# Kernel optimization log

Measured on AMD Instinct MI355X. Metric: run time of the kernel, lower is better.

## Reference

```python
import jax, jax.numpy as jnp
import numpy as np

# Module constants (match init_kwargs)
H = 16            # num_heads
K = 64            # max_kernel_size
MAX_FREQ = 16.0
MIN_FREQ = 1.0
HALF_S = 16       # int(32**(1/1)) // 2
S = 2 * HALF_S + 1  # 33 sample offsets: -16..16
MAX_RECEPTIVE = HALF_S * MAX_FREQ  # 256.0


def setup_inputs() -> dict:
    key = jax.random.key(0)
    ks = jax.random.split(key, 6)
    B, L, C = 1, 4096, 1024
    x = jax.random.normal(ks[0], (B, L, C), dtype=jnp.float32)
    # Learned params (random small scale so offsets/kernels vary; torch inits
    # wave_proj to zeros but that degenerates the math under test).
    Ww = jax.random.normal(ks[1], (2 * H, C), dtype=jnp.float32) * 0.02
    bw = jnp.zeros((2 * H,), dtype=jnp.float32)
    Wk = jax.random.normal(ks[2], (H * K, C), dtype=jnp.float32) * 0.02
    bk = jnp.zeros((H * K,), dtype=jnp.float32)
    Wo = jax.random.normal(ks[3], (C, C), dtype=jnp.float32) * 0.02
    return {"x": x, "Ww": Ww, "bw": bw, "Wk": Wk, "bk": bk, "Wo": Wo}


def reference(x, Ww, bw, Wk, bk, Wo):
    B, L, C = x.shape
    D = C // H
    dt = x.dtype
    grid = jnp.arange(-HALF_S, HALF_S + 1, dtype=dt)  # (S,)

    # Predict per-position frequency / phase (averaged over heads)
    wp = jax.nn.silu(x @ Ww.T + bw).reshape(B, L, 2, H)
    freq = jax.nn.sigmoid(wp[:, :, 0]) * (MAX_FREQ - MIN_FREQ) + MIN_FREQ  # (B,L,H)
    phase = jnp.tanh(wp[:, :, 1]) * MAX_FREQ
    freq_avg = freq.mean(-1)    # (B,L)
    phase_avg = phase.mean(-1)  # (B,L)

    # Sample positions & gather indices
    rel_pos = grid[None, None, :] * freq_avg[..., None] + phase_avg[..., None]  # (B,L,S)
    centers = jnp.arange(L, dtype=dt)
    sample_pos = centers[None, :, None] + rel_pos                               # (B,L,S)
    valid = (sample_pos >= 0) & (sample_pos < L)
    sample_idx = jnp.clip(sample_pos.astype(jnp.int32), 0, L - 1)               # trunc toward 0, like torch .long()

    # Gather values: (B,L,S,C) -> (B,L,H,S,D)
    values = jax.vmap(lambda xf, idx: xf[idx])(x, sample_idx)
    values = values.reshape(B, L, S, H, D).transpose(0, 1, 3, 2, 4)

    # Kernel profile, linearly interpolated to sample positions
    kernel_max = jax.nn.silu(x @ Wk.T + bk).reshape(B, L, H, K)
    norm_pos = jnp.clip((rel_pos + MAX_RECEPTIVE) / (2.0 * MAX_RECEPTIVE), 0.0, 1.0)
    idx_float = norm_pos * (K - 1)                       # (B,L,S)
    idx_floor = jnp.clip(idx_float.astype(jnp.int32), 0, K - 2)
    w_ceil = (idx_float - idx_floor.astype(dt))[:, :, None, :]  # (B,L,1,S)
    w_floor = 1.0 - w_ceil
    ifl = jnp.broadcast_to(idx_floor[:, :, None, :], (B, L, H, S))
    k_floor = jnp.take_along_axis(kernel_max, ifl, axis=-1)
    k_ceil = jnp.take_along_axis(kernel_max, ifl + 1, axis=-1)
    kernel = (k_floor * w_floor + k_ceil * w_ceil) * valid[:, :, None, :].astype(dt)
    kernel = kernel / (kernel.sum(-1, keepdims=True) + 1e-8)

    out = jnp.einsum('blhsd,blhs->blhd', values, kernel).reshape(B, L, C)
    out = jax.nn.silu(out @ Wo.T)
    return out
```

## Files before the change

kernel.cpp:

```cpp
#include <hip/hip_runtime.h>
#include <math.h>

#define LDIM 4096
#define CDIM 1024
#define HDIM 16
#define KDIM 64
#define SDIM 33
#define HALF_SS 16
#define MAXF 16.0f
#define MINF 1.0f
#define MAXR 256.0f

typedef double d4 __attribute__((ext_vector_type(4)));

#define MFMA_F64 __builtin_amdgcn_mfma_f64_16x16x4f64

__device__ __forceinline__ float sigmoid_np(float z) {
  float e = (float)exp(-(double)z);
  return __fdiv_rn(1.0f, __fadd_rn(1.0f, e));
}
__device__ __forceinline__ float silu_f(float z) {
  return __fmul_rn(z, sigmoid_np(z));
}

__device__ __forceinline__ float np_pairwise_sum(const float* a, int n) {
  float r[8];
#pragma unroll
  for (int j = 0; j < 8; ++j) r[j] = a[j];
  int i = 8;
  for (; i + 8 <= n; i += 8)
#pragma unroll
    for (int j = 0; j < 8; ++j) r[j] = __fadd_rn(r[j], a[i + j]);
  float res = __fadd_rn(__fadd_rn(__fadd_rn(r[0], r[1]), __fadd_rn(r[2], r[3])),
                        __fadd_rn(__fadd_rn(r[4], r[5]), __fadd_rn(r[6], r[7])));
  for (; i < n; ++i) res = __fadd_rn(res, a[i]);
  return res;
}

__global__ __launch_bounds__(256) void wave_kernel(
    const float* __restrict__ x, const float* __restrict__ Ww,
    const float* __restrict__ bw, float* __restrict__ fa, float* __restrict__ pa) {
  __shared__ float xs[CDIM];
  __shared__ float wp[2 * HDIM];
  int l = blockIdx.x;
  int tid = threadIdx.x;
  const float* xrow = x + (size_t)l * CDIM;
  for (int c = tid; c < CDIM; c += 256) xs[c] = xrow[c];
  __syncthreads();
  int j = tid >> 3, sub = tid & 7;
  const float* wrow = Ww + j * CDIM;
  double acc = 0.0;
  for (int c = sub; c < CDIM; c += 8) acc += (double)xs[c] * (double)wrow[c];
  for (int off = 4; off; off >>= 1) acc += __shfl_down(acc, off, 8);
  if (sub == 0) {
    float v32 = (float)(acc + (double)bw[j]);
    wp[j] = silu_f(v32);
  }
  __syncthreads();
  if (tid == 0) {
    float fv[HDIM], pv[HDIM];
    for (int h = 0; h < HDIM; ++h) {
      fv[h] = __fadd_rn(__fmul_rn(sigmoid_np(wp[h]), MAXF - MINF), MINF);
      float t32 = (float)tanh((double)wp[HDIM + h]);
      pv[h] = __fmul_rn(t32, MAXF);
    }
    fa[l] = __fdiv_rn(np_pairwise_sum(fv, HDIM), (float)HDIM);
    pa[l] = __fdiv_rn(np_pairwise_sum(pv, HDIM), (float)HDIM);
  }
}

__global__ __launch_bounds__(256) void gemm_bt_silu_f64(
    const float* __restrict__ A, const float* __restrict__ B,
    const float* __restrict__ bias, float* __restrict__ Cout,
    int M, int N, int Kd) {
  __shared__ float Asf[128][36];
  __shared__ float Bsf[64][36];
  int tid = threadIdx.x;
  int w  = tid >> 6;
  int l  = tid & 63;
  int m0 = blockIdx.y * 128, n0 = blockIdx.x * 64;

  d4 zv = (d4)(0.0);
  double lane_d = (double)l;
  d4 pA = MFMA_F64(lane_d, 1.0, zv, 0, 0, 0);
  d4 pB = MFMA_F64(1.0, lane_d, zv, 0, 0, 0);
  int sa0 = (int)pA[0], sb0 = (int)pB[0];
  bool aH1 = ((sa0 & 3) == 0);
  bool bH1 = ((sb0 & 3) == 0);
  int lmA = aH1 ? (l & 15) : (l >> 2);
  int lqA = aH1 ? (l >> 4) : (l & 3);
  int lmB = bH1 ? (l & 15) : (l >> 2);
  int lqB = bH1 ? (l >> 4) : (l & 3);
  int di[4], dj[4];
#pragma unroll
  for (int r = 0; r < 4; ++r) {
    int va = (int)pA[r], vb = (int)pB[r];
    di[r] = (aH1 ? ((va - 96) >> 2) : ((va - 6) >> 4)) & 15;
    dj[r] = (bH1 ? ((vb - 96) >> 2) : ((vb - 6) >> 4)) & 15;
  }

  d4 acc[8];
#pragma unroll
  for (int i = 0; i < 8; ++i) acc[i] = (d4)(0.0);

  for (int kt = 0; kt < Kd; kt += 32) {
#pragma unroll
    for (int qi = 0; qi < 4; ++qi) {
      int e = tid + 256 * qi;
      int row = e >> 3, j = e & 7;
      float4 v = *(const float4*)(A + (size_t)(m0 + row) * Kd + kt + 4 * j);
      Asf[row][j] = v.x; Asf[row][j + 8] = v.y;
      Asf[row][j + 16] = v.z; Asf[row][j + 24] = v.w;
    }
#pragma unroll
    for (int qi = 0; qi < 2; ++qi) {
      int e = tid + 256 * qi;
      int row = e >> 3, j = e & 7;
      float4 v = *(const float4*)(B + (size_t)(n0 + row) * Kd + kt + 4 * j);
      Bsf[row][j] = v.x; Bsf[row][j + 8] = v.y;
      Bsf[row][j + 16] = v.z; Bsf[row][j + 24] = v.w;
    }
    __syncthreads();
#pragma unroll
    for (int t = 0; t < 2; ++t) {
      float4 bv = *(const float4*)&Bsf[16 * w + lmB][8 * lqB + 4 * t];
      float4 av0 = *(const float4*)&Asf[lmA][8 * lqA + 4 * t];
      float4 av1 = *(const float4*)&Asf[16 + lmA][8 * lqA + 4 * t];
      float4 av2 = *(const float4*)&Asf[32 + lmA][8 * lqA + 4 * t];
      float4 av3 = *(const float4*)&Asf[48 + lmA][8 * lqA + 4 * t];
      float4 av4 = *(const float4*)&Asf[64 + lmA][8 * lqA + 4 * t];
      float4 av5 = *(const float4*)&Asf[80 + lmA][8 * lqA + 4 * t];
      float4 av6 = *(const float4*)&Asf[96 + lmA][8 * lqA + 4 * t];
      float4 av7 = *(const float4*)&Asf[112 + lmA][8 * lqA + 4 * t];
      float bs[4] = {bv.x, bv.y, bv.z, bv.w};
      float as0[4] = {av0.x, av0.y, av0.z, av0.w};
      float as1[4] = {av1.x, av1.y, av1.z, av1.w};
      float as2[4] = {av2.x, av2.y, av2.z, av2.w};
      float as3[4] = {av3.x, av3.y, av3.z, av3.w};
      float as4[4] = {av4.x, av4.y, av4.z, av4.w};
      float as5[4] = {av5.x, av5.y, av5.z, av5.w};
      float as6[4] = {av6.x, av6.y, av6.z, av6.w};
      float as7[4] = {av7.x, av7.y, av7.z, av7.w};
#pragma unroll
      for (int s = 0; s < 4; ++s) {
        double bd = (double)bs[s];
        acc[0] = MFMA_F64((double)as0[s], bd, acc[0], 0, 0, 0);
        acc[1] = MFMA_F64((double)as1[s], bd, acc[1], 0, 0, 0);
        acc[2] = MFMA_F64((double)as2[s], bd, acc[2], 0, 0, 0);
        acc[3] = MFMA_F64((double)as3[s], bd, acc[3], 0, 0, 0);
        acc[4] = MFMA_F64((double)as4[s], bd, acc[4], 0, 0, 0);
        acc[5] = MFMA_F64((double)as5[s], bd, acc[5], 0, 0, 0);
        acc[6] = MFMA_F64((double)as6[s], bd, acc[6], 0, 0, 0);
        acc[7] = MFMA_F64((double)as7[s], bd, acc[7], 0, 0, 0);
      }
    }
    __syncthreads();
  }

#pragma unroll
  for (int mt = 0; mt < 8; ++mt) {
#pragma unroll
    for (int r = 0; r < 4; ++r) {
      int mm = m0 + 16 * mt + di[r];
      int nn = n0 + 16 * w + dj[r];
      float v32 = (float)acc[mt][r];
      v32 = __fadd_rn(v32, bias[nn]);
      Cout[(size_t)mm * N + nn] = silu_f(v32);
    }
  }
}

__global__ __launch_bounds__(256) void gemm_bt_silu_f32(
    const float* __restrict__ A, const float* __restrict__ B,
    float* __restrict__ Cout, int M, int N, int Kd) {
  __shared__ float Asf[16][128];
  __shared__ float Bsf[16][128];
  int tid = threadIdx.x;
  int tx = tid & 15, ty = tid >> 4;
  int m0 = blockIdx.y * 128, n0 = blockIdx.x * 128;
  float acc[8][8] = {};
  for (int kt = 0; kt < Kd; kt += 16) {
#pragma unroll
    for (int q = 0; q < 2; ++q) {
      int e = tid + 256 * q;
      int row = e >> 2, kq = (e & 3) * 4;
      float4 va = *(const float4*)(A + (size_t)(m0 + row) * Kd + kt + kq);
      Asf[kq + 0][row] = va.x; Asf[kq + 1][row] = va.y;
      Asf[kq + 2][row] = va.z; Asf[kq + 3][row] = va.w;
      float4 vb = *(const float4*)(B + (size_t)(n0 + row) * Kd + kt + kq);
      Bsf[kq + 0][row] = vb.x; Bsf[kq + 1][row] = vb.y;
      Bsf[kq + 2][row] = vb.z; Bsf[kq + 3][row] = vb.w;
    }
    __syncthreads();
#pragma unroll
    for (int kk = 0; kk < 16; ++kk) {
      float4 a0 = *(const float4*)&Asf[kk][ty * 8];
      float4 a1 = *(const float4*)&Asf[kk][ty * 8 + 4];
      float4 b0 = *(const float4*)&Bsf[kk][tx * 8];
      float4 b1 = *(const float4*)&Bsf[kk][tx * 8 + 4];
      float a[8] = {a0.x, a0.y, a0.z, a0.w, a1.x, a1.y, a1.z, a1.w};
      float b[8] = {b0.x, b0.y, b0.z, b0.w, b1.x, b1.y, b1.z, b1.w};
#pragma unroll
      for (int i = 0; i < 8; ++i)
#pragma unroll
        for (int j2 = 0; j2 < 8; ++j2) acc[i][j2] += a[i] * b[j2];
    }
    __syncthreads();
  }
#pragma unroll
  for (int i = 0; i < 8; ++i) {
    int mm = m0 + ty * 8 + i;
#pragma unroll
    for (int j2 = 0; j2 < 8; ++j2) {
      int nn = n0 + tx * 8 + j2;
      Cout[(size_t)mm * N + nn] = silu_f(acc[i][j2]);
    }
  }
}

__global__ __launch_bounds__(256) void conv_kernel(
    const float* __restrict__ x, const float* __restrict__ km,
    const float* __restrict__ fa, const float* __restrict__ pa,
    float* __restrict__ conv) {
  int l = blockIdx.x;
  int tid = threadIdx.x;
  __shared__ int s_idx[SDIM];
  __shared__ int s_ifl[SDIM];
  __shared__ float s_wc[SDIM];
  __shared__ float s_val[SDIM];
  __shared__ float kern[HDIM][SDIM];
  __shared__ float s_den[HDIM];
  if (tid < SDIM) {
    float f = fa[l], p = pa[l];
    float rel = __fadd_rn(__fmul_rn((float)(tid - HALF_SS), f), p);
    float pos = __fadd_rn((float)l, rel);
    bool valid = (pos >= 0.f) && (pos < (float)LDIM);
    int idx = (int)pos;
    idx = min(max(idx, 0), LDIM - 1);
    s_idx[tid] = idx;
    s_val[tid] = valid ? 1.f : 0.f;
    float np_ = __fdiv_rn(__fadd_rn(rel, MAXR), 2.f * MAXR);
    np_ = fminf(fmaxf(np_, 0.f), 1.f);
    float idxf = __fmul_rn(np_, (float)(KDIM - 1));
    int ifl = (int)idxf;
    ifl = min(max(ifl, 0), KDIM - 2);
    s_ifl[tid] = ifl;
    s_wc[tid] = __fsub_rn(idxf, (float)ifl);
  }
  __syncthreads();
  for (int t = tid; t < HDIM * SDIM; t += 256) {
    int h = t / SDIM, s = t - h * SDIM;
    const float* kb = km + (size_t)l * CDIM + h * KDIM;
    float wc = s_wc[s];
    float wf = __fsub_rn(1.f, wc);
    float v = __fadd_rn(__fmul_rn(kb[s_ifl[s]], wf), __fmul_rn(kb[s_ifl[s] + 1], wc));
    kern[h][s] = __fmul_rn(v, s_val[s]);
  }
  __syncthreads();
  if (tid < HDIM) {
    float sum = np_pairwise_sum(&kern[tid][0], SDIM);
    s_den[tid] = __fadd_rn(sum, 1e-8f);
  }
  __syncthreads();
  for (int t = tid; t < HDIM * SDIM; t += 256) {
    int h = t / SDIM, s = t - h * SDIM;
    kern[h][s] = __fdiv_rn(kern[h][s], s_den[h]);
  }
  __syncthreads();
  float acc[4] = {0.f, 0.f, 0.f, 0.f};
  for (int s = 0; s < SDIM; ++s) {
    const float* xr = x + (size_t)s_idx[s] * CDIM;
#pragma unroll
    for (int q = 0; q < 4; ++q) {
      int c = tid + q * 256;
      acc[q] = __fadd_rn(acc[q], __fmul_rn(xr[c], kern[c >> 6][s]));
    }
  }
#pragma unroll
  for (int q = 0; q < 4; ++q) {
    int c = tid + q * 256;
    conv[(size_t)l * CDIM + c] = acc[q];
  }
}

extern "C" void kernel_launch(void* const* d_in, const int* in_sizes, int n_in,
                              void* d_out, int out_size, void* d_ws, size_t ws_size,
                              hipStream_t stream) {
  const float* x  = (const float*)d_in[0];
  const float* Ww = (const float*)d_in[1];
  const float* bw = (const float*)d_in[2];
  const float* Wk = (const float*)d_in[3];
  const float* bk = (const float*)d_in[4];
  const float* Wo = (const float*)d_in[5];
  float* out = (float*)d_out;

  float* fa   = (float*)d_ws;
  float* pa   = fa + LDIM;
  float* km   = pa + LDIM;
  float* conv = km + (size_t)LDIM * CDIM;

  wave_kernel<<<LDIM, 256, 0, stream>>>(x, Ww, bw, fa, pa);

  dim3 kmgrid(CDIM / 64, LDIM / 128);
  gemm_bt_silu_f64<<<kmgrid, 256, 0, stream>>>(x, Wk, bk, km, LDIM, CDIM, CDIM);

  conv_kernel<<<LDIM, 256, 0, stream>>>(x, km, fa, pa, conv);

  dim3 ogrid(CDIM / 128, LDIM / 128);
  gemm_bt_silu_f32<<<ogrid, 256, 0, stream>>>(conv, Wo, out, LDIM, CDIM, CDIM);
}
```

Baseline: 456.1 us.

## Retile output GEMM to 512 threads, pad LDS, vectorize conv loads and stores

```diff
diff --git a/kernel.cpp b/kernel.cpp
--- a/kernel.cpp
+++ b/kernel.cpp
@@ -170,51 +170,51 @@
   }
 }
 
-__global__ __launch_bounds__(256) void gemm_bt_silu_f32(
+__global__ __launch_bounds__(512) void gemm_bt_silu_f32(
     const float* __restrict__ A, const float* __restrict__ B,
     float* __restrict__ Cout, int M, int N, int Kd) {
-  __shared__ float Asf[16][128];
-  __shared__ float Bsf[16][128];
+  __shared__ float Asf[16][132];
+  __shared__ float Bsf[16][132];
   int tid = threadIdx.x;
-  int tx = tid & 15, ty = tid >> 4;
+  int tx = tid & 15;
+  int ty = tid >> 4;
   int m0 = blockIdx.y * 128, n0 = blockIdx.x * 128;
-  float acc[8][8] = {};
+  float acc[4][8] = {};
+  int rS = tid >> 2, kq = (tid & 3) * 4;
   for (int kt = 0; kt < Kd; kt += 16) {
-#pragma unroll
-    for (int q = 0; q < 2; ++q) {
-      int e = tid + 256 * q;
-      int row = e >> 2, kq = (e & 3) * 4;
-      float4 va = *(const float4*)(A + (size_t)(m0 + row) * Kd + kt + kq);
-      Asf[kq + 0][row] = va.x; Asf[kq + 1][row] = va.y;
-      Asf[kq + 2][row] = va.z; Asf[kq + 3][row] = va.w;
-      float4 vb = *(const float4*)(B + (size_t)(n0 + row) * Kd + kt + kq);
-      Bsf[kq + 0][row] = vb.x; Bsf[kq + 1][row] = vb.y;
-      Bsf[kq + 2][row] = vb.z; Bsf[kq + 3][row] = vb.w;
+    {
+      float4 va = *(const float4*)(A + (size_t)(m0 + rS) * Kd + kt + kq);
+      Asf[kq + 0][rS] = va.x; Asf[kq + 1][rS] = va.y;
+      Asf[kq + 2][rS] = va.z; Asf[kq + 3][rS] = va.w;
+      float4 vb = *(const float4*)(B + (size_t)(n0 + rS) * Kd + kt + kq);
+      Bsf[kq + 0][rS] = vb.x; Bsf[kq + 1][rS] = vb.y;
+      Bsf[kq + 2][rS] = vb.z; Bsf[kq + 3][rS] = vb.w;
     }
     __syncthreads();
 #pragma unroll
     for (int kk = 0; kk < 16; ++kk) {
-      float4 a0 = *(const float4*)&Asf[kk][ty * 8];
-      float4 a1 = *(const float4*)&Asf[kk][ty * 8 + 4];
-      float4 b0 = *(const float4*)&Bsf[kk][tx * 8];
-      float4 b1 = *(const float4*)&Bsf[kk][tx * 8 + 4];
-      float a[8] = {a0.x, a0.y, a0.z, a0.w, a1.x, a1.y, a1.z, a1.w};
+      float4 a0 = *(const float4*)&Asf[kk][ty * 4];
+      float4 b0 = *(const float4*)&Bsf[kk][tx * 4];
+      float4 b1 = *(const float4*)&Bsf[kk][tx * 4 + 64];
+      float a[4] = {a0.x, a0.y, a0.z, a0.w};
       float b[8] = {b0.x, b0.y, b0.z, b0.w, b1.x, b1.y, b1.z, b1.w};
 #pragma unroll
-      for (int i = 0; i < 8; ++i)
+      for (int i = 0; i < 4; ++i)
 #pragma unroll
         for (int j2 = 0; j2 < 8; ++j2) acc[i][j2] += a[i] * b[j2];
     }
     __syncthreads();
   }
 #pragma unroll
-  for (int i = 0; i < 8; ++i) {
-    int mm = m0 + ty * 8 + i;
-#pragma unroll
-    for (int j2 = 0; j2 < 8; ++j2) {
-      int nn = n0 + tx * 8 + j2;
-      Cout[(size_t)mm * N + nn] = silu_f(acc[i][j2]);
-    }
+  for (int i = 0; i < 4; ++i) {
+    int mm = m0 + ty * 4 + i;
+    float4 o0, o1;
+    o0.x = silu_f(acc[i][0]); o0.y = silu_f(acc[i][1]);
+    o0.z = silu_f(acc[i][2]); o0.w = silu_f(acc[i][3]);
+    o1.x = silu_f(acc[i][4]); o1.y = silu_f(acc[i][5]);
+    o1.z = silu_f(acc[i][6]); o1.w = silu_f(acc[i][7]);
+    *(float4*)&Cout[(size_t)mm * N + n0 + 4 * tx] = o0;
+    *(float4*)&Cout[(size_t)mm * N + n0 + 64 + 4 * tx] = o1;
   }
 }
 
@@ -222,7 +222,8 @@
     const float* __restrict__ x, const float* __restrict__ km,
     const float* __restrict__ fa, const float* __restrict__ pa,
     float* __restrict__ conv) {
-  int l = blockIdx.x;
+  int bid = blockIdx.x;
+  int l = (bid & 7) * (LDIM / 8) + (bid >> 3);
   int tid = threadIdx.x;
   __shared__ int s_idx[SDIM];
   __shared__ int s_ifl[SDIM];
@@ -267,20 +268,20 @@
     kern[h][s] = __fdiv_rn(kern[h][s], s_den[h]);
   }
   __syncthreads();
-  float acc[4] = {0.f, 0.f, 0.f, 0.f};
+  int c0 = tid * 4;
+  int h0 = c0 >> 6;
+  float acc0 = 0.f, acc1 = 0.f, acc2 = 0.f, acc3 = 0.f;
   for (int s = 0; s < SDIM; ++s) {
-    const float* xr = x + (size_t)s_idx[s] * CDIM;
-#pragma unroll
-    for (int q = 0; q < 4; ++q) {
-      int c = tid + q * 256;
-      acc[q] = __fadd_rn(acc[q], __fmul_rn(xr[c], kern[c >> 6][s]));
-    }
-  }
-#pragma unroll
-  for (int q = 0; q < 4; ++q) {
-    int c = tid + q * 256;
-    conv[(size_t)l * CDIM + c] = acc[q];
-  }
+    float4 xv = *(const float4*)(x + (size_t)s_idx[s] * CDIM + c0);
+    float kv = kern[h0][s];
+    acc0 = __fadd_rn(acc0, __fmul_rn(xv.x, kv));
+    acc1 = __fadd_rn(acc1, __fmul_rn(xv.y, kv));
+    acc2 = __fadd_rn(acc2, __fmul_rn(xv.z, kv));
+    acc3 = __fadd_rn(acc3, __fmul_rn(xv.w, kv));
+  }
+  float4 o;
+  o.x = acc0; o.y = acc1; o.z = acc2; o.w = acc3;
+  *(float4*)&conv[(size_t)l * CDIM + c0] = o;
 }
 
 extern "C" void kernel_launch(void* const* d_in, const int* in_sizes, int n_in,
@@ -307,5 +308,5 @@
   conv_kernel<<<LDIM, 256, 0, stream>>>(x, km, fa, pa, conv);
 
   dim3 ogrid(CDIM / 128, LDIM / 128);
-  gemm_bt_silu_f32<<<ogrid, 256, 0, stream>>>(conv, Wo, out, LDIM, CDIM, CDIM);
-}
+  gemm_bt_silu_f32<<<ogrid, 512, 0, stream>>>(conv, Wo, out, LDIM, CDIM, CDIM);
+}
```

Result: faster. 434.5 us (-4.7%).
